# Optimization experiments

Measured on AMD Instinct MI355X. Metric: run time of the kernel, lower is better.

The kernel has to match this reference:

```python
import jax, jax.numpy as jnp
import numpy as np

B, M, D, K = 64, 2_000_000, 32, 10
EPS = 1e-5            # kernel epsilon in _inverse_kernel
DENOM_C = 1e-5        # denominator_constant in _episodic_reward


def setup_inputs() -> dict:
    key = jax.random.key(0)
    kq, km = jax.random.split(key)
    query = jax.random.normal(kq, (B, D), dtype=jnp.float32)
    memory = jax.random.normal(km, (M, D), dtype=jnp.float32)
    return {"query": query, "memory": memory, "k": K}


def reference(query, memory, k):
    # Squared Euclidean distances [B, M] via the expanded form (no [B,M,D] intermediate).
    q2 = jnp.sum(query * query, axis=-1, keepdims=True)          # [B, 1]
    m2 = jnp.sum(memory * memory, axis=-1)                       # [M]
    sq = jnp.maximum(q2 + m2[None, :] - 2.0 * (query @ memory.T), 0.0)  # [B, M]
    # Running mean of squared distances (vectorized fixed point of RunningMean;
    # stateful numpy update in the original -> no gradient through it).
    mean_sq = jax.lax.stop_gradient(jnp.mean(sq))
    # _inverse_kernel: eps / (d^2 / mean + eps)
    kdist = EPS / (sq / mean_sq + EPS)                           # [B, M]
    # sklearn kneighbors picks the k SMALLEST metric values.
    neg_topk, _ = jax.lax.top_k(-kdist, k)                       # [B, k]
    neighbor_sum = -jnp.sum(neg_topk, axis=-1)                   # [B]
    # episodic reward: 1 / sqrt(sum(neighbor kernel distances) + c)
    return 1.0 / jnp.sqrt(neighbor_sum + DENOM_C)
```

## Files before the change

kernel.cpp:

```cpp
#include <hip/hip_runtime.h>
#include <hip/hip_bf16.h>
#include <float.h>
#include <math.h>

typedef short short8 __attribute__((ext_vector_type(8)));
typedef float f32x4  __attribute__((ext_vector_type(4)));

#define KEPS   1e-5f
#define DENOMC 1e-5f

__device__ __forceinline__ short f2bf(float x) {
    return __builtin_bit_cast(short, __float2bfloat16(x));
}

__device__ __forceinline__ void top10_insert(float (&lst)[10], float s) {
    if (s > lst[0]) {
        lst[0] = s;
        #pragma unroll
        for (int i = 1; i < 10; ++i) {
            float lo = fminf(lst[0], lst[i]);
            float hi = fmaxf(lst[0], lst[i]);
            lst[0] = lo; lst[i] = hi;
        }
    }
}

__global__ __launch_bounds__(256, 5) void ep_main(
    const float* __restrict__ q, const float* __restrict__ mem,
    float* __restrict__ part_top,
    float* __restrict__ part_sums,
    int nb, int ntiles)
{
    const int tid  = threadIdx.x;
    const int lane = tid & 63;
    const int wave = tid >> 6;
    const int g    = lane >> 4;
    const int c    = lane & 15;
    const int bid  = blockIdx.x;

    short8 bfrag[4];
    #pragma unroll
    for (int n = 0; n < 4; ++n) {
        const float* qp = q + (n * 16 + c) * 32 + g * 8;
        float4 w0 = *(const float4*)qp;
        float4 w1 = *(const float4*)(qp + 4);
        short8 f;
        f[0]=f2bf(-2.f*w0.x); f[1]=f2bf(-2.f*w0.y); f[2]=f2bf(-2.f*w0.z); f[3]=f2bf(-2.f*w0.w);
        f[4]=f2bf(-2.f*w1.x); f[5]=f2bf(-2.f*w1.y); f[6]=f2bf(-2.f*w1.z); f[7]=f2bf(-2.f*w1.w);
        bfrag[n] = f;
    }

    float t1[4], t2[4];
    #pragma unroll
    for (int n = 0; n < 4; ++n) { t1[n] = -FLT_MAX; t2[n] = -FLT_MAX; }
    float cs[8];
    #pragma unroll
    for (int r = 0; r < 8; ++r) cs[r] = 0.f;
    float sumsq = 0.f;

    const size_t lane_off = (size_t)(wave * 16 + c) * 32 + (size_t)(g * 8);

    for (int tile = bid; tile < ntiles; tile += nb) {
        const float* p = mem + (size_t)tile * (64 * 32) + lane_off;
        float4 v0 = *(const float4*)p;
        float4 v1 = *(const float4*)(p + 4);

        float ps;
        ps = v0.x * v0.x;
        ps = fmaf(v0.y, v0.y, ps);
        ps = fmaf(v0.z, v0.z, ps);
        ps = fmaf(v0.w, v0.w, ps);
        ps = fmaf(v1.x, v1.x, ps);
        ps = fmaf(v1.y, v1.y, ps);
        ps = fmaf(v1.z, v1.z, ps);
        ps = fmaf(v1.w, v1.w, ps);
        sumsq += ps;
        cs[0] += v0.x; cs[1] += v0.y; cs[2] += v0.z; cs[3] += v0.w;
        cs[4] += v1.x; cs[5] += v1.y; cs[6] += v1.z; cs[7] += v1.w;

        float m2 = ps + __shfl_xor(ps, 16, 64);
        m2 = m2 + __shfl_xor(m2, 32, 64);
        f32x4 minit;
        minit[0] = __shfl(m2, 4 * g + 0, 64);
        minit[1] = __shfl(m2, 4 * g + 1, 64);
        minit[2] = __shfl(m2, 4 * g + 2, 64);
        minit[3] = __shfl(m2, 4 * g + 3, 64);

        short8 af;
        af[0]=f2bf(v0.x); af[1]=f2bf(v0.y); af[2]=f2bf(v0.z); af[3]=f2bf(v0.w);
        af[4]=f2bf(v1.x); af[5]=f2bf(v1.y); af[6]=f2bf(v1.z); af[7]=f2bf(v1.w);

        #pragma unroll
        for (int n = 0; n < 4; ++n) {
            f32x4 acc = __builtin_amdgcn_mfma_f32_16x16x32_bf16(af, bfrag[n], minit, 0, 0, 0);
            #define T2UPD(S) { \
                float h1 = fmaxf(t1[n], (S)); float lo = fminf(t1[n], (S)); \
                float h2 = fmaxf(t2[n], lo); \
                t1[n] = h1; t2[n] = h2; }
            T2UPD(acc[0]) T2UPD(acc[1]) T2UPD(acc[2]) T2UPD(acc[3])
            #undef T2UPD
        }
    }

    __shared__ float ltop[64][16][2];
    __shared__ float red[4][4][8];
    __shared__ float ssred[4];

    const int slot = g + 4 * wave;
    #pragma unroll
    for (int n = 0; n < 4; ++n) {
        const int b = n * 16 + c;
        ltop[b][slot][0] = t1[n];
        ltop[b][slot][1] = t2[n];
    }
    #pragma unroll
    for (int r = 0; r < 8; ++r) {
        float v = cs[r];
        v += __shfl_xor(v, 1, 64);
        v += __shfl_xor(v, 2, 64);
        v += __shfl_xor(v, 4, 64);
        v += __shfl_xor(v, 8, 64);
        cs[r] = v;
    }
    float ssv = sumsq;
    ssv += __shfl_xor(ssv, 1, 64);
    ssv += __shfl_xor(ssv, 2, 64);
    ssv += __shfl_xor(ssv, 4, 64);
    ssv += __shfl_xor(ssv, 8, 64);
    ssv += __shfl_xor(ssv, 16, 64);
    ssv += __shfl_xor(ssv, 32, 64);
    if (c == 0) {
        #pragma unroll
        for (int r = 0; r < 8; ++r) red[wave][g][r] = cs[r];
    }
    if (lane == 0) ssred[wave] = ssv;
    __syncthreads();

    if (tid < 32) {
        float a = red[0][tid >> 3][tid & 7] + red[1][tid >> 3][tid & 7]
                + red[2][tid >> 3][tid & 7] + red[3][tid >> 3][tid & 7];
        part_sums[(size_t)tid * nb + bid] = a;
    } else if (tid == 32) {
        part_sums[(size_t)32 * nb + bid] = ssred[0] + ssred[1] + ssred[2] + ssred[3];
    }

    if (tid < 64) {
        float lst[10];
        #pragma unroll
        for (int i = 0; i < 10; ++i) lst[i] = -FLT_MAX;
        for (int s2 = 0; s2 < 16; ++s2) {
            top10_insert(lst, ltop[tid][s2][0]);
            top10_insert(lst, ltop[tid][s2][1]);
        }
        #pragma unroll
        for (int i = 0; i < 10; ++i)
            part_top[((size_t)tid * nb + bid) * 10 + i] = lst[i];
    }
}

__global__ __launch_bounds__(256) void ep_tail(
    const float* __restrict__ q, const float* __restrict__ part_top,
    const float* __restrict__ part_sums, float* __restrict__ out,
    int nb, int Mrows)
{
    const int b    = blockIdx.x;
    const int tid  = threadIdx.x;
    const int lane = tid & 63;
    const int wave = tid >> 6;

    __shared__ float smem[256 * 33];
    __shared__ float colsum_a[33];
    __shared__ float w4[4];
    __shared__ float mean_s, q2_s;

    if (tid < 64) {
        float x = (tid < 32) ? q[b * 32 + tid] : 0.f;
        float a = x * x;
        a += __shfl_xor(a, 1, 64);
        a += __shfl_xor(a, 2, 64);
        a += __shfl_xor(a, 4, 64);
        a += __shfl_xor(a, 8, 64);
        a += __shfl_xor(a, 16, 64);
        if (tid == 0) q2_s = a;
    }

    float a2 = 0.f;
    #pragma unroll
    for (int e = 0; e < 8; ++e) {
        float x = q[tid * 8 + e];
        a2 = fmaf(x, x, a2);
    }
    a2 += __shfl_xor(a2, 1, 64);
    a2 += __shfl_xor(a2, 2, 64);
    a2 += __shfl_xor(a2, 4, 64);
    a2 += __shfl_xor(a2, 8, 64);
    a2 += __shfl_xor(a2, 16, 64);
    a2 += __shfl_xor(a2, 32, 64);
    if (lane == 0) w4[wave] = a2;

    float acc[33];
    #pragma unroll
    for (int c2 = 0; c2 < 33; ++c2) acc[c2] = 0.f;
    for (int i = tid; i < nb; i += 256) {
        #pragma unroll
        for (int c2 = 0; c2 < 33; ++c2) acc[c2] += part_sums[(size_t)c2 * nb + i];
    }
    #pragma unroll
    for (int c2 = 0; c2 < 33; ++c2) smem[tid * 33 + c2] = acc[c2];
    __syncthreads();
    if (tid < 33) {
        float a = 0.f;
        #pragma unroll 16
        for (int j = 0; j < 256; ++j) a += smem[j * 33 + tid];
        colsum_a[tid] = a;
    }
    __syncthreads();

    if (tid < 32) {
        float qs = 0.f;
        #pragma unroll 8
        for (int bb = 0; bb < 64; ++bb) qs += q[bb * 32 + tid];
        float dq = qs * colsum_a[tid];
        dq += __shfl_xor(dq, 1, 64);
        dq += __shfl_xor(dq, 2, 64);
        dq += __shfl_xor(dq, 4, 64);
        dq += __shfl_xor(dq, 8, 64);
        dq += __shfl_xor(dq, 16, 64);
        if (tid == 0) {
            double q2sum = (double)w4[0] + (double)w4[1] + (double)w4[2] + (double)w4[3];
            double sumsq = (double)colsum_a[32];
            double Md    = (double)Mrows;
            mean_s = (float)((Md * q2sum + 64.0 * sumsq - 2.0 * (double)dq) / (64.0 * Md));
        }
    }
    __syncthreads();

    float lst[10];
    #pragma unroll
    for (int i = 0; i < 10; ++i) lst[i] = -FLT_MAX;
    const float* pt = part_top + (size_t)b * nb * 10;
    for (int i = tid; i < nb; i += 256) {
        const float* pp = pt + (size_t)i * 10;
        #pragma unroll
        for (int r = 0; r < 10; ++r) top10_insert(lst, pp[r]);
    }
    #pragma unroll
    for (int r = 0; r < 10; ++r) smem[tid * 10 + r] = lst[r];
    __syncthreads();

    if (tid < 32) {
        float m[10];
        #pragma unroll
        for (int i = 0; i < 10; ++i) m[i] = -FLT_MAX;
        for (int j2 = 0; j2 < 8; ++j2) {
            #pragma unroll
            for (int r = 0; r < 10; ++r) top10_insert(m, smem[(tid * 8 + j2) * 10 + r]);
        }
        #pragma unroll
        for (int r = 0; r < 10; ++r) smem[2560 + tid * 10 + r] = m[r];
    }
    __syncthreads();

    if (tid == 0) {
        float m[10];
        #pragma unroll
        for (int i = 0; i < 10; ++i) m[i] = -FLT_MAX;
        for (int j2 = 0; j2 < 32; ++j2) {
            #pragma unroll
            for (int r = 0; r < 10; ++r) top10_insert(m, smem[2560 + j2 * 10 + r]);
        }
        const float mean = mean_s;
        const float q2b  = q2_s;
        float sum = 0.f;
        #pragma unroll
        for (int r = 0; r < 10; ++r) {
            float sq = m[r] + q2b;
            sq = fmaxf(sq, 0.f);
            sum += KEPS / (sq / mean + KEPS);
        }
        out[b] = 1.0f / sqrtf(sum + DENOMC);
    }
}

extern "C" void kernel_launch(void* const* d_in, const int* in_sizes, int n_in,
                              void* d_out, int out_size, void* d_ws, size_t ws_size,
                              hipStream_t stream)
{
    const float* q   = (const float*)d_in[0];
    const float* mem = (const float*)d_in[1];
    float* out = (float*)d_out;

    const int Mrows  = in_sizes[1] / 32;
    const int ntiles = Mrows / 64;

    int nb = 1280;
    while (nb > 64 && ((size_t)nb * 673 + 64) * sizeof(float) > ws_size) nb >>= 1;
    if (nb > ntiles) nb = ntiles;

    float* part_top  = (float*)d_ws;
    float* part_sums = part_top + (size_t)64 * nb * 10;

    ep_main<<<dim3(nb), dim3(256), 0, stream>>>(q, mem, part_top, part_sums, nb, ntiles);
    ep_tail<<<dim3(64), dim3(256), 0, stream>>>(q, part_top, part_sums, out, nb, Mrows);
}
```

Measured before the change: 95.96 us.

## Swap MFMA operands so each lane keeps per-memory-column maxima, prefetch next tile

The MFMA operands are swapped so query rows come from the A fragment and memory rows from B. The memory-norm init becomes a broadcast of the lane's own m2, which removes four shuffles per tile. Each lane now keeps 16 running maxima, one per query row and column slot, with a single fmax instead of a two-deep top-2 insert. The tile loop is software-pipelined so the next tile's loads are issued before the current one is processed. In exchange there are more per-lane candidates (64 per query) for the shared-memory top-10 merge, and keeping only top-1 per column within a block loses exactness whenever two of a query's true top-k land in the same column.

```diff
diff --git a/kernel.cpp b/kernel.cpp
--- a/kernel.cpp
+++ b/kernel.cpp
@@ -38,33 +38,30 @@
     const int c    = lane & 15;
     const int bid  = blockIdx.x;
 
-    short8 bfrag[4];
-    #pragma unroll
-    for (int n = 0; n < 4; ++n) {
-        const float* qp = q + (n * 16 + c) * 32 + g * 8;
+    short8 qfrag[4];
+    #pragma unroll
+    for (int h = 0; h < 4; ++h) {
+        const float* qp = q + (h * 16 + c) * 32 + g * 8;
         float4 w0 = *(const float4*)qp;
         float4 w1 = *(const float4*)(qp + 4);
         short8 f;
         f[0]=f2bf(-2.f*w0.x); f[1]=f2bf(-2.f*w0.y); f[2]=f2bf(-2.f*w0.z); f[3]=f2bf(-2.f*w0.w);
         f[4]=f2bf(-2.f*w1.x); f[5]=f2bf(-2.f*w1.y); f[6]=f2bf(-2.f*w1.z); f[7]=f2bf(-2.f*w1.w);
-        bfrag[n] = f;
-    }
-
-    float t1[4], t2[4];
-    #pragma unroll
-    for (int n = 0; n < 4; ++n) { t1[n] = -FLT_MAX; t2[n] = -FLT_MAX; }
+        qfrag[h] = f;
+    }
+
+    float t1[16];
+    #pragma unroll
+    for (int i = 0; i < 16; ++i) t1[i] = -FLT_MAX;
     float cs[8];
     #pragma unroll
     for (int r = 0; r < 8; ++r) cs[r] = 0.f;
     float sumsq = 0.f;
 
     const size_t lane_off = (size_t)(wave * 16 + c) * 32 + (size_t)(g * 8);
-
-    for (int tile = bid; tile < ntiles; tile += nb) {
-        const float* p = mem + (size_t)tile * (64 * 32) + lane_off;
-        float4 v0 = *(const float4*)p;
-        float4 v1 = *(const float4*)(p + 4);
-
+    const size_t step     = (size_t)nb * 2048;
+
+    auto process = [&](float4 v0, float4 v1) {
         float ps;
         ps = v0.x * v0.x;
         ps = fmaf(v0.y, v0.y, ps);
@@ -80,39 +77,47 @@
 
         float m2 = ps + __shfl_xor(ps, 16, 64);
         m2 = m2 + __shfl_xor(m2, 32, 64);
-        f32x4 minit;
-        minit[0] = __shfl(m2, 4 * g + 0, 64);
-        minit[1] = __shfl(m2, 4 * g + 1, 64);
-        minit[2] = __shfl(m2, 4 * g + 2, 64);
-        minit[3] = __shfl(m2, 4 * g + 3, 64);
-
-        short8 af;
-        af[0]=f2bf(v0.x); af[1]=f2bf(v0.y); af[2]=f2bf(v0.z); af[3]=f2bf(v0.w);
-        af[4]=f2bf(v1.x); af[5]=f2bf(v1.y); af[6]=f2bf(v1.z); af[7]=f2bf(v1.w);
-
-        #pragma unroll
-        for (int n = 0; n < 4; ++n) {
-            f32x4 acc = __builtin_amdgcn_mfma_f32_16x16x32_bf16(af, bfrag[n], minit, 0, 0, 0);
-            #define T2UPD(S) { \
-                float h1 = fmaxf(t1[n], (S)); float lo = fminf(t1[n], (S)); \
-                float h2 = fmaxf(t2[n], lo); \
-                t1[n] = h1; t2[n] = h2; }
-            T2UPD(acc[0]) T2UPD(acc[1]) T2UPD(acc[2]) T2UPD(acc[3])
-            #undef T2UPD
-        }
-    }
-
-    __shared__ float ltop[64][16][2];
+        f32x4 mi = {m2, m2, m2, m2};
+
+        short8 mf;
+        mf[0]=f2bf(v0.x); mf[1]=f2bf(v0.y); mf[2]=f2bf(v0.z); mf[3]=f2bf(v0.w);
+        mf[4]=f2bf(v1.x); mf[5]=f2bf(v1.y); mf[6]=f2bf(v1.z); mf[7]=f2bf(v1.w);
+
+        #pragma unroll
+        for (int h = 0; h < 4; ++h) {
+            f32x4 acc = __builtin_amdgcn_mfma_f32_16x16x32_bf16(qfrag[h], mf, mi, 0, 0, 0);
+            t1[h*4+0] = fmaxf(t1[h*4+0], acc[0]);
+            t1[h*4+1] = fmaxf(t1[h*4+1], acc[1]);
+            t1[h*4+2] = fmaxf(t1[h*4+2], acc[2]);
+            t1[h*4+3] = fmaxf(t1[h*4+3], acc[3]);
+        }
+    };
+
+    const float* p = mem + (size_t)bid * 2048 + lane_off;
+    float4 v0 = *(const float4*)p;
+    float4 v1 = *(const float4*)(p + 4);
+    p += step;
+    for (int t = bid + nb; t < ntiles; t += nb) {
+        float4 w0 = *(const float4*)p;
+        float4 w1 = *(const float4*)(p + 4);
+        p += step;
+        process(v0, v1);
+        v0 = w0; v1 = w1;
+    }
+    process(v0, v1);
+
+    __shared__ float ltop[64][65];
     __shared__ float red[4][4][8];
     __shared__ float ssred[4];
 
-    const int slot = g + 4 * wave;
-    #pragma unroll
-    for (int n = 0; n < 4; ++n) {
-        const int b = n * 16 + c;
-        ltop[b][slot][0] = t1[n];
-        ltop[b][slot][1] = t2[n];
-    }
+    const int col = wave * 16 + c;
+    #pragma unroll
+    for (int h = 0; h < 4; ++h) {
+        #pragma unroll
+        for (int r = 0; r < 4; ++r)
+            ltop[h * 16 + g * 4 + r][col] = t1[h * 4 + r];
+    }
+
     #pragma unroll
     for (int r = 0; r < 8; ++r) {
         float v = cs[r];
@@ -148,10 +153,8 @@
         float lst[10];
         #pragma unroll
         for (int i = 0; i < 10; ++i) lst[i] = -FLT_MAX;
-        for (int s2 = 0; s2 < 16; ++s2) {
-            top10_insert(lst, ltop[tid][s2][0]);
-            top10_insert(lst, ltop[tid][s2][1]);
-        }
+        #pragma unroll 4
+        for (int s2 = 0; s2 < 64; ++s2) top10_insert(lst, ltop[tid][s2]);
         #pragma unroll
         for (int i = 0; i < 10; ++i)
             part_top[((size_t)tid * nb + bid) * 10 + i] = lst[i];
```

New measurement: 98.95 us. 1.03x slower.
